# Performance work log

Measured on AMD Instinct MI355X. Metric: run time of the kernel, lower is better.

The kernel has to match this reference:

```python
import jax, jax.numpy as jnp
import numpy as np

N = 100000
E = 1600000
F_IN = 128
H = 128


def setup_inputs() -> dict:
    key = jax.random.key(0)
    ks = jax.random.split(key, 12)
    x = jax.random.normal(ks[0], (N, F_IN), dtype=jnp.float32)
    edge_index = jax.random.randint(ks[1], (2, E), 0, N, dtype=jnp.int64)
    s = 1.0 / np.sqrt(F_IN)
    sh = 1.0 / np.sqrt(H)
    inp = {"x": x, "edge_index": edge_index}
    # SAGEConv params: lin_l (neighbor agg, with bias), lin_r (root, no bias)
    inp["W1l"] = jax.random.uniform(ks[2], (H, F_IN), jnp.float32, -s, s)
    inp["b1"] = jnp.zeros((H,), jnp.float32)
    inp["W1r"] = jax.random.uniform(ks[3], (H, F_IN), jnp.float32, -s, s)
    inp["W2l"] = jax.random.uniform(ks[4], (H, H), jnp.float32, -sh, sh)
    inp["b2"] = jnp.zeros((H,), jnp.float32)
    inp["W2r"] = jax.random.uniform(ks[5], (H, H), jnp.float32, -sh, sh)
    inp["W3l"] = jax.random.uniform(ks[6], (H, H), jnp.float32, -sh, sh)
    inp["b3"] = jnp.zeros((H,), jnp.float32)
    inp["W3r"] = jax.random.uniform(ks[7], (H, H), jnp.float32, -sh, sh)
    inp["Wo"] = jax.random.uniform(ks[8], (1, H), jnp.float32, -sh, sh)
    inp["bo"] = jnp.zeros((1,), jnp.float32)
    return inp


def _sage_max(h, src, dst, Wl, bl, Wr):
    # max-aggregate source features at destination nodes (empty -> 0, as PyG)
    m = jax.ops.segment_max(h[src], dst, num_segments=N)  # [N, d]
    m = jnp.where(jnp.isfinite(m), m, jnp.zeros_like(m))
    return m @ Wl.T + bl + h @ Wr.T


def reference(x, edge_index, W1l, b1, W1r, W2l, b2, W2r, W3l, b3, W3r, Wo, bo):
    src, dst = edge_index[0], edge_index[1]
    h1 = jax.nn.elu(_sage_max(x, src, dst, W1l, b1, W1r))
    h2 = jax.nn.elu(_sage_max(h1, src, dst, W2l, b2, W2r)) + h1
    h3 = jax.nn.elu(_sage_max(h2, src, dst, W3l, b3, W3r)) + h2
    return jax.nn.sigmoid(h3 @ Wo.T + bo)  # [N, 1]
```

## Files before the change

kernel.cpp:

```cpp
#include <hip/hip_runtime.h>
#include <hip/hip_fp16.h>
#include <math.h>

#define HDIM 128

#define BSHIFT 7
#define BW 128
#define BCAP 4096
#define NBKMAX 1024
#define CHUNK 4096

typedef __attribute__((ext_vector_type(8))) _Float16 f16x8;
typedef __attribute__((ext_vector_type(2))) _Float16 f16x2;
typedef __attribute__((ext_vector_type(16))) float f32x16;
typedef unsigned int uint32;
typedef unsigned short u16;

__device__ __forceinline__ uint32 hmax2u(uint32 a, uint32 b) {
    f16x2 ha = __builtin_bit_cast(f16x2, a);
    f16x2 hb = __builtin_bit_cast(f16x2, b);
    f16x2 r = __builtin_elementwise_max(ha, hb);
    return __builtin_bit_cast(uint32, r);
}
__device__ __forceinline__ uint32 hadd2u(uint32 a, uint32 b) {
    f16x2 ha = __builtin_bit_cast(f16x2, a);
    f16x2 hb = __builtin_bit_cast(f16x2, b);
    f16x2 r = ha + hb;
    return __builtin_bit_cast(uint32, r);
}


__global__ __launch_bounds__(256) void bucket_bin(
    const int* __restrict__ ei, int E_, int nbk,
    int* __restrict__ bucketCnt, uint32* __restrict__ tmp)
{
    __shared__ int cnt[NBKMAX];
    __shared__ int gbase[NBKMAX];
    const int t = threadIdx.x;
    const int start = blockIdx.x * CHUNK;
    const int end = min(start + CHUNK, E_);

    for (int i = t; i < nbk; i += 256) cnt[i] = 0;
    __syncthreads();
    for (int e = start + t; e < end; e += 256)
        atomicAdd(&cnt[ei[E_ + e] >> BSHIFT], 1);
    __syncthreads();
    for (int i = t; i < nbk; i += 256) {
        int c = cnt[i];
        gbase[i] = c ? atomicAdd(&bucketCnt[i], c) : 0;
    }
    __syncthreads();
    for (int i = t; i < nbk; i += 256) cnt[i] = 0;
    __syncthreads();
    for (int e = start + t; e < end; e += 256) {
        int d = ei[E_ + e];
        int s = ei[e];
        int b = d >> BSHIFT;
        int r = atomicAdd(&cnt[b], 1);
        tmp[(size_t)b * BCAP + gbase[b] + r] =
            ((uint32)(d & (BW - 1)) << 17) | (uint32)s;
    }
}

__global__ __launch_bounds__(1024) void bucket_scan(
    const int* __restrict__ bucketCnt, int* __restrict__ bucketBase,
    int nbk, int* __restrict__ off, int N_, int E_) {
    __shared__ int sd[1024];
    int t = threadIdx.x;
    int v = (t < nbk) ? bucketCnt[t] : 0;
    sd[t] = v;
    __syncthreads();
    for (int ofs = 1; ofs < 1024; ofs <<= 1) {
        int add = (t >= ofs) ? sd[t - ofs] : 0;
        __syncthreads();
        sd[t] += add;
        __syncthreads();
    }
    if (t < nbk) bucketBase[t] = sd[t] - v;
    if (t == 0) off[N_] = E_;
}

__global__ __launch_bounds__(256) void bucket_csr(
    const uint32* __restrict__ tmp, const int* __restrict__ bucketCnt,
    const int* __restrict__ bucketBase,
    int* __restrict__ off, int* __restrict__ srcs, int N_)
{
    __shared__ int lc[BW];
    __shared__ int lo[BW];
    __shared__ int sd[256];
    const int b = blockIdx.x, t = threadIdx.x;
    const int cnt = bucketCnt[b], base = bucketBase[b];
    const uint32* tp = tmp + (size_t)b * BCAP;

    if (t < BW) lc[t] = 0;
    __syncthreads();
    for (int i = t; i < cnt; i += 256) atomicAdd(&lc[tp[i] >> 17], 1);
    __syncthreads();

    int v = (t < BW) ? lc[t] : 0;
    sd[t] = v;
    __syncthreads();
    for (int ofs = 1; ofs < 256; ofs <<= 1) {
        int add = (t >= ofs) ? sd[t - ofs] : 0;
        __syncthreads();
        sd[t] += add;
        __syncthreads();
    }
    if (t < BW) lo[t] = sd[t] - v;
    __syncthreads();

    for (int i = t; i < BW; i += 256) {
        int node = b * BW + i;
        if (node < N_) off[node] = base + lo[i];
    }
    if (t < BW) lc[t] = lo[t];
    __syncthreads();
    for (int i = t; i < cnt; i += 256) {
        uint32 p = tp[i];
        int dl = p >> 17, s = p & 0x1FFFF;
        int pos = base + atomicAdd(&lc[dl], 1);
        srcs[pos] = s;
    }
}


__global__ void cast_x(const float* __restrict__ x, uint32* __restrict__ xb, int n2) {
    int i = blockIdx.x * 256 + threadIdx.x;
    if (i >= n2) return;
    float2 v = ((const float2*)x)[i];
    f16x2 h = { (_Float16)v.x, (_Float16)v.y };
    xb[i] = __builtin_bit_cast(uint32, h);
}

__global__ void cast_weights_packed(
    const float* __restrict__ W1l, const float* __restrict__ W1r,
    const float* __restrict__ W2l, const float* __restrict__ W2r,
    const float* __restrict__ W3l, const float* __restrict__ W3r,
    f16x8* __restrict__ PW)
{
    int tid = blockIdx.x * 256 + threadIdx.x;
    if (tid >= 3 * 4096) return;
    int layer = tid >> 12, rem = tid & 4095;
    int g = rem >> 10, ks = (rem >> 6) & 15, lane = rem & 63;
    int col = g * 32 + (lane & 31), kq = lane >> 5;
    const float* src;
    if (layer == 0)      src = (ks < 8) ? W1l : W1r;
    else if (layer == 1) src = (ks < 8) ? W2l : W2r;
    else                 src = (ks < 8) ? W3l : W3r;
    int kk = (ks & 7) * 16 + kq * 8;
    f16x8 v;
#pragma unroll
    for (int j = 0; j < 8; ++j) v[j] = (_Float16)src[col * HDIM + kk + j];
    PW[tid] = v;
}


__global__ __launch_bounds__(256) void gather_max(
    const uint32* __restrict__ hb,
    uint32* __restrict__ mb,
    const int* __restrict__ off, const int* __restrict__ srcs, int n_nodes)
{
    const int w = threadIdx.x >> 6, lane = threadIdx.x & 63;
    const int node = blockIdx.x * 4 + w;
    if (node >= n_nodes) return;
    const int es = lane >> 4, ch = lane & 15;
    const int e0 = off[node], e1 = off[node + 1];
    const uint4* hp = (const uint4*)hb;

    const uint32 NINF = 0xFC00FC00u;
    uint32 m0 = NINF, m1 = NINF, m2 = NINF, m3 = NINF;

    int e = e0 + es;
    for (; e + 12 < e1; e += 16) {
        int s0 = srcs[e], s1 = srcs[e + 4], s2 = srcs[e + 8], s3 = srcs[e + 12];
        uint4 v0 = hp[(size_t)s0 * 16 + ch];
        uint4 v1 = hp[(size_t)s1 * 16 + ch];
        uint4 v2 = hp[(size_t)s2 * 16 + ch];
        uint4 v3 = hp[(size_t)s3 * 16 + ch];
        m0 = hmax2u(m0, v0.x); m1 = hmax2u(m1, v0.y);
        m2 = hmax2u(m2, v0.z); m3 = hmax2u(m3, v0.w);
        m0 = hmax2u(m0, v1.x); m1 = hmax2u(m1, v1.y);
        m2 = hmax2u(m2, v1.z); m3 = hmax2u(m3, v1.w);
        m0 = hmax2u(m0, v2.x); m1 = hmax2u(m1, v2.y);
        m2 = hmax2u(m2, v2.z); m3 = hmax2u(m3, v2.w);
        m0 = hmax2u(m0, v3.x); m1 = hmax2u(m1, v3.y);
        m2 = hmax2u(m2, v3.z); m3 = hmax2u(m3, v3.w);
    }
    for (; e < e1; e += 4) {
        uint4 v0 = hp[(size_t)srcs[e] * 16 + ch];
        m0 = hmax2u(m0, v0.x); m1 = hmax2u(m1, v0.y);
        m2 = hmax2u(m2, v0.z); m3 = hmax2u(m3, v0.w);
    }

    m0 = hmax2u(m0, __shfl_xor(m0, 16)); m0 = hmax2u(m0, __shfl_xor(m0, 32));
    m1 = hmax2u(m1, __shfl_xor(m1, 16)); m1 = hmax2u(m1, __shfl_xor(m1, 32));
    m2 = hmax2u(m2, __shfl_xor(m2, 16)); m2 = hmax2u(m2, __shfl_xor(m2, 32));
    m3 = hmax2u(m3, __shfl_xor(m3, 16)); m3 = hmax2u(m3, __shfl_xor(m3, 32));

    if (es == 0) {
        uint4 r = make_uint4(0u, 0u, 0u, 0u);
        if (e1 > e0) { r.x = m0; r.y = m1; r.z = m2; r.w = m3; }
        ((uint4*)mb)[(size_t)node * 16 + ch] = r;
    }
}


#define ESTRIDE 136

__global__ __launch_bounds__(256) void gemm_layer(
    const uint4* __restrict__ mb, const uint4* __restrict__ hb,
    const uint4* __restrict__ res, uint4* __restrict__ outb,
    const uint4* __restrict__ PW,
    const float* __restrict__ bias, int n_nodes)
{
    __shared__ uint4 sm[512];
    __shared__ uint4 sh[512];
    __shared__ _Float16 ho[32 * ESTRIDE];
    const int t = threadIdx.x, lane = t & 63, w = t >> 6;
    const int base = blockIdx.x * 32;
    const int l31 = lane & 31, kq = lane >> 5;

#pragma unroll
    for (int r = 0; r < 2; ++r) {
        int g = r * 256 + t;
        int row = g >> 4, ch = g & 15;
        int sw = ch ^ (row & 7);
        size_t gi = (size_t)(base + row) * 16 + ch;
        sm[row * 16 + sw] = mb[gi];
        sh[row * 16 + sw] = hb[gi];
    }
    __syncthreads();

    f32x16 acc = {};

#pragma unroll
    for (int k = 0; k < 8; ++k) {
        f16x8 a = __builtin_bit_cast(f16x8, sm[l31 * 16 + ((2 * k + kq) ^ (l31 & 7))]);
        f16x8 b = __builtin_bit_cast(f16x8, PW[(w * 16 + k) * 64 + lane]);
        acc = __builtin_amdgcn_mfma_f32_32x32x16_f16(a, b, acc, 0, 0, 0);
    }
#pragma unroll
    for (int k = 0; k < 8; ++k) {
        f16x8 a = __builtin_bit_cast(f16x8, sh[l31 * 16 + ((2 * k + kq) ^ (l31 & 7))]);
        f16x8 b = __builtin_bit_cast(f16x8, PW[(w * 16 + 8 + k) * 64 + lane]);
        acc = __builtin_amdgcn_mfma_f32_32x32x16_f16(a, b, acc, 0, 0, 0);
    }

    const int C = w * 32 + l31;
    const float bv = bias[C];
#pragma unroll
    for (int r = 0; r < 16; ++r) {
        int row = (r & 3) + 8 * (r >> 2) + 4 * kq;
        float v = acc[r] + bv;
        v = (v > 0.f) ? v : (__expf(v) - 1.f);
        ho[row * ESTRIDE + C] = (_Float16)v;
    }
    __syncthreads();

#pragma unroll
    for (int r = 0; r < 2; ++r) {
        int g = r * 256 + t;
        int row = g >> 4, ch = g & 15;
        int R = base + row;
        if (R >= n_nodes) continue;
        uint4 v = *(const uint4*)&ho[row * ESTRIDE + ch * 8];
        if (res) {
            uint4 rv = res[(size_t)R * 16 + ch];
            v.x = hadd2u(v.x, rv.x); v.y = hadd2u(v.y, rv.y);
            v.z = hadd2u(v.z, rv.z); v.w = hadd2u(v.w, rv.w);
        }
        outb[(size_t)R * 16 + ch] = v;
    }
}


__global__ __launch_bounds__(256) void readout(
    const uint32* __restrict__ h, const float* __restrict__ Wo,
    const float* __restrict__ bo, float* __restrict__ out, int n_nodes)
{
    int t = threadIdx.x;
    int n = t >> 4, l = t & 15;
    int node = blockIdx.x * 16 + n;
    if (node >= n_nodes) return;
    float s = 0.f;
    for (int j = l; j < 64; j += 16) {
        uint32 v = h[(size_t)node * 64 + j];
        f16x2 hh = __builtin_bit_cast(f16x2, v);
        s += (float)hh.x * Wo[2 * j] + (float)hh.y * Wo[2 * j + 1];
    }
    for (int o = 8; o; o >>= 1) s += __shfl_down(s, o, 16);
    if (l == 0) out[node] = 1.f / (1.f + expf(-(s + bo[0])));
}


extern "C" void kernel_launch(void* const* d_in, const int* in_sizes, int n_in,
                              void* d_out, int out_size, void* d_ws, size_t ws_size,
                              hipStream_t stream) {
    const float* x   = (const float*)d_in[0];
    const int*   ei  = (const int*)d_in[1];
    const float* W1l = (const float*)d_in[2];
    const float* b1  = (const float*)d_in[3];
    const float* W1r = (const float*)d_in[4];
    const float* W2l = (const float*)d_in[5];
    const float* b2  = (const float*)d_in[6];
    const float* W2r = (const float*)d_in[7];
    const float* W3l = (const float*)d_in[8];
    const float* b3  = (const float*)d_in[9];
    const float* W3r = (const float*)d_in[10];
    const float* Wo  = (const float*)d_in[11];
    const float* bo  = (const float*)d_in[12];
    float* out = (float*)d_out;

    const int N_ = in_sizes[0] / HDIM;
    const int E_ = in_sizes[1] / 2;
    const int Np = (N_ + 127) & ~127;
    const int nbk = (N_ + BW - 1) / BW;

    size_t o = 0;
    auto carve = [&](size_t bytes) { size_t r = o; o = (o + bytes + 255) & ~255ULL; return r; };
    char* ws = (char*)d_ws;
    int* off        = (int*)(ws + carve((size_t)(N_ + 1) * 4));
    int* bucketCnt  = (int*)(ws + carve((size_t)NBKMAX * 4));
    int* bucketBase = (int*)(ws + carve((size_t)NBKMAX * 4));
    int* srcs       = (int*)(ws + carve((size_t)E_ * 4));
    uint32* tmp     = (uint32*)(ws + carve((size_t)nbk * BCAP * 4));
    uint4* PW       = (uint4*)(ws + carve((size_t)3 * 4096 * 16));
    uint32* XB      = (uint32*)(ws + carve((size_t)Np * 64 * 4));
    uint32* H1B     = (uint32*)(ws + carve((size_t)Np * 64 * 4));
    uint32* MB      = (uint32*)(ws + carve((size_t)Np * 64 * 4));
    (void)ws_size; (void)n_in; (void)out_size;

    (void)hipMemsetAsync(bucketCnt, 0, (size_t)NBKMAX * 4, stream);
    bucket_bin<<<(E_ + CHUNK - 1) / CHUNK, 256, 0, stream>>>(ei, E_, nbk, bucketCnt, tmp);
    bucket_scan<<<1, 1024, 0, stream>>>(bucketCnt, bucketBase, nbk, off, N_, E_);
    bucket_csr<<<nbk, 256, 0, stream>>>(tmp, bucketCnt, bucketBase, off, srcs, N_);

    cast_weights_packed<<<(3 * 4096 + 255) / 256, 256, 0, stream>>>(
        W1l, W1r, W2l, W2r, W3l, W3r, (f16x8*)PW);
    cast_x<<<(N_ * 64 + 255) / 256, 256, 0, stream>>>(x, XB, N_ * 64);

    const int nbG = (N_ + 3) / 4;
    const int nbM = Np / 32;

    const uint4* PW1 = PW;
    const uint4* PW2 = PW + 4096;
    const uint4* PW3 = PW + 8192;

    gather_max<<<nbG, 256, 0, stream>>>(XB, MB, off, srcs, N_);
    gemm_layer<<<nbM, 256, 0, stream>>>((const uint4*)MB, (const uint4*)XB, nullptr,
                                        (uint4*)H1B, PW1, b1, N_);
    gather_max<<<nbG, 256, 0, stream>>>(H1B, MB, off, srcs, N_);
    gemm_layer<<<nbM, 256, 0, stream>>>((const uint4*)MB, (const uint4*)H1B, (const uint4*)H1B,
                                        (uint4*)XB, PW2, b2, N_);
    gather_max<<<nbG, 256, 0, stream>>>(XB, MB, off, srcs, N_);
    gemm_layer<<<nbM, 256, 0, stream>>>((const uint4*)MB, (const uint4*)XB, (const uint4*)XB,
                                        (uint4*)H1B, PW3, b3, N_);

    readout<<<(N_ + 15) / 16, 256, 0, stream>>>(H1B, Wo, bo, out, N_);
}
```

Baseline: 402.0 us.

## Split gather_max feature dimension across 8 blocks with edge-parallel lanes

The max-aggregation kernel now splits each node's 128-feature row into 8 chunks of 16 halves, each handled by a separate block, and spreads 16 edges across a wavefront's lanes (4 lanes per edge, 8 bytes each) instead of 4 edges with 16-byte loads. This gives more independent edges in flight per node to hide gather latency for low-degree nodes, and the launch grid grows eightfold. The trade-off is narrower 8-byte loads, offsets and source indices read eight times, more shuffle reduction steps, and more blocks to schedule.

```diff
diff --git a/kernel.cpp b/kernel.cpp
--- a/kernel.cpp
+++ b/kernel.cpp
@@ -160,47 +160,42 @@
     uint32* __restrict__ mb,
     const int* __restrict__ off, const int* __restrict__ srcs, int n_nodes)
 {
+    const int chunk = blockIdx.x & 7;
+    const int ng = blockIdx.x >> 3;
     const int w = threadIdx.x >> 6, lane = threadIdx.x & 63;
-    const int node = blockIdx.x * 4 + w;
+    const int node = ng * 4 + w;
     if (node >= n_nodes) return;
-    const int es = lane >> 4, ch = lane & 15;
+    const int q = lane & 3;
+    const int es = lane >> 2;
     const int e0 = off[node], e1 = off[node + 1];
-    const uint4* hp = (const uint4*)hb;
+    const uint2* hp = (const uint2*)hb;
+    const int coff = chunk * 4 + q;
 
     const uint32 NINF = 0xFC00FC00u;
-    uint32 m0 = NINF, m1 = NINF, m2 = NINF, m3 = NINF;
+    uint32 m0 = NINF, m1 = NINF;
 
     int e = e0 + es;
-    for (; e + 12 < e1; e += 16) {
-        int s0 = srcs[e], s1 = srcs[e + 4], s2 = srcs[e + 8], s3 = srcs[e + 12];
-        uint4 v0 = hp[(size_t)s0 * 16 + ch];
-        uint4 v1 = hp[(size_t)s1 * 16 + ch];
-        uint4 v2 = hp[(size_t)s2 * 16 + ch];
-        uint4 v3 = hp[(size_t)s3 * 16 + ch];
+    for (; e + 16 < e1; e += 32) {
+        int s0 = srcs[e], s1 = srcs[e + 16];
+        uint2 v0 = hp[(size_t)s0 * 32 + coff];
+        uint2 v1 = hp[(size_t)s1 * 32 + coff];
         m0 = hmax2u(m0, v0.x); m1 = hmax2u(m1, v0.y);
-        m2 = hmax2u(m2, v0.z); m3 = hmax2u(m3, v0.w);
         m0 = hmax2u(m0, v1.x); m1 = hmax2u(m1, v1.y);
-        m2 = hmax2u(m2, v1.z); m3 = hmax2u(m3, v1.w);
-        m0 = hmax2u(m0, v2.x); m1 = hmax2u(m1, v2.y);
-        m2 = hmax2u(m2, v2.z); m3 = hmax2u(m3, v2.w);
-        m0 = hmax2u(m0, v3.x); m1 = hmax2u(m1, v3.y);
-        m2 = hmax2u(m2, v3.z); m3 = hmax2u(m3, v3.w);
-    }
-    for (; e < e1; e += 4) {
-        uint4 v0 = hp[(size_t)srcs[e] * 16 + ch];
+    }
+    if (e < e1) {
+        uint2 v0 = hp[(size_t)srcs[e] * 32 + coff];
         m0 = hmax2u(m0, v0.x); m1 = hmax2u(m1, v0.y);
-        m2 = hmax2u(m2, v0.z); m3 = hmax2u(m3, v0.w);
-    }
-
-    m0 = hmax2u(m0, __shfl_xor(m0, 16)); m0 = hmax2u(m0, __shfl_xor(m0, 32));
-    m1 = hmax2u(m1, __shfl_xor(m1, 16)); m1 = hmax2u(m1, __shfl_xor(m1, 32));
-    m2 = hmax2u(m2, __shfl_xor(m2, 16)); m2 = hmax2u(m2, __shfl_xor(m2, 32));
-    m3 = hmax2u(m3, __shfl_xor(m3, 16)); m3 = hmax2u(m3, __shfl_xor(m3, 32));
+    }
+
+    m0 = hmax2u(m0, __shfl_xor(m0, 4));  m1 = hmax2u(m1, __shfl_xor(m1, 4));
+    m0 = hmax2u(m0, __shfl_xor(m0, 8));  m1 = hmax2u(m1, __shfl_xor(m1, 8));
+    m0 = hmax2u(m0, __shfl_xor(m0, 16)); m1 = hmax2u(m1, __shfl_xor(m1, 16));
+    m0 = hmax2u(m0, __shfl_xor(m0, 32)); m1 = hmax2u(m1, __shfl_xor(m1, 32));
 
     if (es == 0) {
-        uint4 r = make_uint4(0u, 0u, 0u, 0u);
-        if (e1 > e0) { r.x = m0; r.y = m1; r.z = m2; r.w = m3; }
-        ((uint4*)mb)[(size_t)node * 16 + ch] = r;
+        uint2 r = make_uint2(0u, 0u);
+        if (e1 > e0) { r.x = m0; r.y = m1; }
+        ((uint2*)mb)[(size_t)node * 32 + coff] = r;
     }
 }
 
@@ -339,7 +334,7 @@
         W1l, W1r, W2l, W2r, W3l, W3r, (f16x8*)PW);
     cast_x<<<(N_ * 64 + 255) / 256, 256, 0, stream>>>(x, XB, N_ * 64);
 
-    const int nbG = (N_ + 3) / 4;
+    const int nbG = ((N_ + 3) / 4) * 8;
     const int nbM = Np / 32;
 
     const uint4* PW1 = PW;
```

After: 904.6 us. 125% more time.
